# Kernel optimization log

Measured on AMD Instinct MI355X. Metric: run time of the kernel, lower is better.

Reference implementation:

```python
import jax, jax.numpy as jnp
import numpy as np

EPS = 1e-5
SLOPE = 0.2

def lrelu(x):
    return jnp.where(x > 0, x, SLOPE * x)

def bn_train(x, gamma, beta, axes):
    # training-mode batch norm over `axes`, channel dim = 1 (or features dim for 2D input)
    mean = jnp.mean(x, axis=axes, keepdims=True)
    var = jnp.mean((x - mean) ** 2, axis=axes, keepdims=True)
    sh = [1] * x.ndim
    sh[1] = -1
    return gamma.reshape(sh) * (x - mean) * jax.lax.rsqrt(var + EPS) + beta.reshape(sh)

def knn_sum(x, k):
    # x: (B, C, N). k-NN graph via pairwise squared distance, then sum of
    # gathered neighbor features over the k neighbors -> (B, C, N).
    inner = jnp.einsum('bcn,bcm->bnm', x, x)            # (B,N,N)
    sq = jnp.sum(x * x, axis=1)                          # (B,N)
    neg_dist = 2.0 * inner - sq[:, :, None] - sq[:, None, :]
    _, idx = jax.lax.top_k(neg_dist, k)                  # (B,N,k) nearest (incl. self)
    # gather: feat[b,c,n,j] = x[b,c,idx[b,n,j]]
    feat = jnp.take_along_axis(x[:, :, None, :], idx[:, None, :, :], axis=3)  # (B,C,N,k)
    return jnp.sum(feat, axis=3)

def edge_block(x, W, g, b, k):
    # get_graph_feature -> sum over neighbors -> conv1x1 -> BN -> LeakyReLU
    agg = knn_sum(x, k)                                  # (B,C,N)
    y = jnp.einsum('oc,bcn->bon', W, agg)                # 1x1 conv, no bias
    return lrelu(bn_train(y, g, b, (0, 2)))


def setup_inputs() -> dict:
    key = jax.random.key(0)
    ks = jax.random.split(key, 16)
    B, N, E, OUT = 16, 1024, 1024, 40
    w = lambda k_, sh, s=0.05: jax.random.normal(k_, sh, jnp.float32) * s
    ones = lambda n: jnp.ones((n,), jnp.float32)
    zeros = lambda n: jnp.zeros((n,), jnp.float32)
    return {
        'x': jax.random.normal(ks[0], (B, 3, N), jnp.float32),
        'W1': w(ks[1], (64, 3)),   'g1': ones(64),  'b1': zeros(64),
        'W2': w(ks[2], (64, 64)),  'g2': ones(64),  'b2': zeros(64),
        'W3': w(ks[3], (128, 64)), 'g3': ones(128), 'b3': zeros(128),
        'W4': w(ks[4], (256, 128)),'g4': ones(256), 'b4': zeros(256),
        'W5': w(ks[5], (E, 512)),  'g5': ones(E),   'b5': zeros(E),
        'lin1W': w(ks[6], (512, 2 * E)), 'g6': ones(512), 'b6': zeros(512),
        'lin2W': w(ks[7], (256, 512)), 'lin2b': zeros(256), 'g7': ones(256), 'b7': zeros(256),
        'lin3W': w(ks[8], (OUT, 256)), 'lin3b': zeros(OUT),
        'k': 20,
    }


def reference(x, W1, g1, b1, W2, g2, b2, W3, g3, b3, W4, g4, b4,
              W5, g5, b5, lin1W, g6, b6, lin2W, lin2b, g7, b7,
              lin3W, lin3b, k):
    x1 = edge_block(x,  W1, g1, b1, k)   # (B, 64, N)
    x2 = edge_block(x1, W2, g2, b2, k)   # (B, 64, N)
    x3 = edge_block(x2, W3, g3, b3, k)   # (B,128, N)
    x4 = edge_block(x3, W4, g4, b4, k)   # (B,256, N)
    h = jnp.concatenate([x1, x2, x3, x4], axis=1)        # (B,512,N)
    h = lrelu(bn_train(jnp.einsum('oc,bcn->bon', W5, h), g5, b5, (0, 2)))  # (B,E,N)
    hmax = jnp.max(h, axis=2)
    havg = jnp.mean(h, axis=2)
    z = jnp.concatenate([hmax, havg], axis=1)            # (B, 2E)
    z = lrelu(bn_train(z @ lin1W.T, g6, b6, (0,)))
    z = lrelu(bn_train(z @ lin2W.T + lin2b, g7, b7, (0,)))  # dropout = identity (eval)
    return z @ lin3W.T + lin3b                           # (B, 40)
```

## Files before the change

kernel.cpp:

```cpp
#include <hip/hip_runtime.h>
#include <hip/hip_bf16.h>
#include <math.h>

#define NPTS 1024
#define BATCH 16
#define KNN 20

typedef __attribute__((ext_vector_type(8))) short short8;
typedef __attribute__((ext_vector_type(4))) float f32x4;

__global__ __launch_bounds__(256) void compute_sq_kernel(const float* __restrict__ X,
    long batchStride, int C, float* __restrict__ sq) {
  const int b = blockIdx.y;
  const int m = blockIdx.x * 256 + threadIdx.x;
  const float* Xb = X + (long)b * batchStride;
  float s = 0.f;
  for (int c = 0; c < C; ++c) { float v = Xb[(long)c * NPTS + m]; s += v * v; }
  sq[b * NPTS + m] = s;
}

__global__ __launch_bounds__(256) void transpose_split_kernel(const float* __restrict__ in,
    long inBatchStride, int C, unsigned short* __restrict__ XH,
    unsigned short* __restrict__ XM, unsigned short* __restrict__ XL,
    float* __restrict__ XT) {
  __shared__ float tile[64][65];
  const int b  = blockIdx.z;
  const int n0 = blockIdx.x * 64, c0 = blockIdx.y * 64;
  const int tid = threadIdx.x;
  const float* ib = in + (long)b * inBatchStride;
  for (int i = tid; i < 4096; i += 256) {
    int r = i >> 6, cn = i & 63;
    tile[r][cn] = ib[(long)(c0 + r) * NPTS + n0 + cn];
  }
  __syncthreads();
  const long pb = (long)b * ((long)NPTS * C);
  for (int i = tid; i < 4096; i += 256) {
    int r = i >> 6, cc = i & 63;
    float f = tile[cc][r];
    __hip_bfloat16 h = __float2bfloat16(f);
    float r1 = f - __bfloat162float(h);
    __hip_bfloat16 m = __float2bfloat16(r1);
    float r2 = r1 - __bfloat162float(m);
    __hip_bfloat16 l = __float2bfloat16(r2);
    const long o = pb + (long)(n0 + r) * C + c0 + cc;
    XH[o] = *(unsigned short*)&h;
    XM[o] = *(unsigned short*)&m;
    XL[o] = *(unsigned short*)&l;
    XT[o] = f;
  }
}

template<int C>
__global__ __launch_bounds__(256) void knn_mfma_kernel(
    const unsigned short* __restrict__ XH, const unsigned short* __restrict__ XM,
    const unsigned short* __restrict__ XL, const float* __restrict__ sqg,
    float* __restrict__ PARTV, unsigned short* __restrict__ PARTI) {
  __shared__ __align__(16) unsigned short QP[6][64][40];
  __shared__ __align__(16) float Dbuf[64][68];
  float* region = (float*)&QP[0][0][0];

  const int b     = blockIdx.z;
  const int q0    = blockIdx.x * 64;
  const int p0    = blockIdx.y * 256;
  const int chunk = blockIdx.y;
  const int tid  = threadIdx.x;
  const int lane = tid & 63, w = tid >> 6;
  const int l16  = lane & 15, quad = lane >> 4;
  const int q = lane, sub = w;

  const long plane = (long)b * ((long)NPTS * C);
  const unsigned short* XHb = XH + plane;
  const unsigned short* XMb = XM + plane;
  const unsigned short* XLb = XL + plane;

  float sqw[4][4];
  #pragma unroll
  for (int pci = 0; pci < 4; ++pci)
    #pragma unroll
    for (int r = 0; r < 4; ++r)
      sqw[pci][r] = sqg[b * NPTS + p0 + pci * 64 + w * 16 + quad * 4 + r];

  float topv[KNN];
  int   topi[KNN];
  #pragma unroll
  for (int j = 0; j < KNN; ++j) { topv[j] = -INFINITY; topi[j] = 0x7fffffff; }
  float vmin = -INFINITY;

  const int srow = tid >> 2, sseg = (tid & 3) * 8;
  constexpr int KCN = C / 32;

  float4 rg0, rg1, rg2, rg3, rg4, rg5;
  {
    const long qo = (long)(q0 + srow) * C + sseg;
    const long po = (long)(p0 + srow) * C + sseg;
    rg0 = *(const float4*)&XHb[qo];
    rg1 = *(const float4*)&XMb[qo];
    rg2 = *(const float4*)&XLb[qo];
    rg3 = *(const float4*)&XHb[po];
    rg4 = *(const float4*)&XMb[po];
    rg5 = *(const float4*)&XLb[po];
  }

  for (int pci = 0; pci < 4; ++pci) {
    f32x4 acc[4];
    #pragma unroll
    for (int t = 0; t < 4; ++t) acc[t] = (f32x4){0.f, 0.f, 0.f, 0.f};

    for (int kci = 0; kci < KCN; ++kci) {
      __syncthreads();
      *(float4*)&QP[0][srow][sseg] = rg0;
      *(float4*)&QP[1][srow][sseg] = rg1;
      *(float4*)&QP[2][srow][sseg] = rg2;
      *(float4*)&QP[3][srow][sseg] = rg3;
      *(float4*)&QP[4][srow][sseg] = rg4;
      *(float4*)&QP[5][srow][sseg] = rg5;
      __syncthreads();
      const int ns = pci * KCN + kci + 1;
      if (ns < 4 * KCN) {
        const int npc = ns / KCN, nkc = (ns % KCN) * 32;
        const long qo = (long)(q0 + srow) * C + nkc + sseg;
        const long po = (long)(p0 + npc * 64 + srow) * C + nkc + sseg;
        rg0 = *(const float4*)&XHb[qo];
        rg1 = *(const float4*)&XMb[qo];
        rg2 = *(const float4*)&XLb[qo];
        rg3 = *(const float4*)&XHb[po];
        rg4 = *(const float4*)&XMb[po];
        rg5 = *(const float4*)&XLb[po];
      }
      const short8 ph = *(const short8*)&QP[3][w * 16 + l16][quad * 8];
      const short8 pm = *(const short8*)&QP[4][w * 16 + l16][quad * 8];
      const short8 pl = *(const short8*)&QP[5][w * 16 + l16][quad * 8];
      #pragma unroll
      for (int t = 0; t < 4; ++t) {
        const short8 qh = *(const short8*)&QP[0][t * 16 + l16][quad * 8];
        const short8 qm = *(const short8*)&QP[1][t * 16 + l16][quad * 8];
        const short8 ql = *(const short8*)&QP[2][t * 16 + l16][quad * 8];
        acc[t] = __builtin_amdgcn_mfma_f32_16x16x32_bf16(ph, qh, acc[t], 0, 0, 0);
        acc[t] = __builtin_amdgcn_mfma_f32_16x16x32_bf16(ph, qm, acc[t], 0, 0, 0);
        acc[t] = __builtin_amdgcn_mfma_f32_16x16x32_bf16(pm, qh, acc[t], 0, 0, 0);
        acc[t] = __builtin_amdgcn_mfma_f32_16x16x32_bf16(pm, qm, acc[t], 0, 0, 0);
        acc[t] = __builtin_amdgcn_mfma_f32_16x16x32_bf16(ph, ql, acc[t], 0, 0, 0);
        acc[t] = __builtin_amdgcn_mfma_f32_16x16x32_bf16(pl, qh, acc[t], 0, 0, 0);
      }
    }
    #pragma unroll
    for (int t = 0; t < 4; ++t)
      #pragma unroll
      for (int r = 0; r < 4; ++r)
        Dbuf[w * 16 + quad * 4 + r][t * 16 + l16] = fmaf(2.f, acc[t][r], -sqw[pci][r]);
    __syncthreads();

    #pragma unroll 4
    for (int i = 0; i < 16; ++i) {
      const float v = Dbuf[sub * 16 + i][q];
      if (v > vmin) {
        float cv = v; int ci = p0 + pci * 64 + sub * 16 + i;
        bool ins = false;
        #pragma unroll
        for (int j = 0; j < KNN; ++j) {
          const float tv = topv[j]; const int ti = topi[j];
          const bool gt = ins || (cv > tv);
          topv[j] = gt ? cv : tv;
          topi[j] = gt ? ci : ti;
          cv = gt ? tv : cv;
          ci = gt ? ti : ci;
          ins = gt;
        }
        vmin = topv[KNN - 1];
      }
    }
  }

  __syncthreads();
  {
    float* mv = region;
    unsigned short* mi = (unsigned short*)(region + 5120);
    const int slot = q * 4 + sub;
    #pragma unroll
    for (int j = 0; j < KNN; ++j) { mv[j * 256 + slot] = topv[j]; mi[j * 256 + slot] = (unsigned short)topi[j]; }
  }
  __syncthreads();
  if (tid < 64) {
    const float* mv = region;
    const unsigned short* mi = (const unsigned short*)(region + 5120);
    int p0_ = 0, p1 = 0, p2 = 0, p3 = 0;
    float* opv = PARTV + (((long)(b * NPTS + q0 + tid)) * 4 + chunk) * KNN;
    unsigned short* opi = PARTI + (((long)(b * NPTS + q0 + tid)) * 4 + chunk) * KNN;
    for (int j = 0; j < KNN; ++j) {
      float bv = -INFINITY; int bi = 0x7fffffff; int bs = 0;
      if (p0_ < KNN) { float v = mv[p0_ * 256 + tid * 4 + 0]; int i = mi[p0_ * 256 + tid * 4 + 0];
        if (v > bv || (v == bv && i < bi)) { bv = v; bi = i; bs = 0; } }
      if (p1 < KNN) { float v = mv[p1 * 256 + tid * 4 + 1]; int i = mi[p1 * 256 + tid * 4 + 1];
        if (v > bv || (v == bv && i < bi)) { bv = v; bi = i; bs = 1; } }
      if (p2 < KNN) { float v = mv[p2 * 256 + tid * 4 + 2]; int i = mi[p2 * 256 + tid * 4 + 2];
        if (v > bv || (v == bv && i < bi)) { bv = v; bi = i; bs = 2; } }
      if (p3 < KNN) { float v = mv[p3 * 256 + tid * 4 + 3]; int i = mi[p3 * 256 + tid * 4 + 3];
        if (v > bv || (v == bv && i < bi)) { bv = v; bi = i; bs = 3; } }
      p0_ += (bs == 0); p1 += (bs == 1); p2 += (bs == 2); p3 += (bs == 3);
      opv[j] = bv; opi[j] = (unsigned short)bi;
    }
  }
}

template<int C>
__global__ __launch_bounds__(256) void knn_kernel(const float* __restrict__ X,
    long batchStride, const float* __restrict__ sqg,
    float* __restrict__ PARTV, unsigned short* __restrict__ PARTI) {
  constexpr int CT = (C < 64) ? C : 64;
  constexpr int REGF = (2 * CT * 64 > 7680) ? 2 * CT * 64 : 7680;
  __shared__ float Dbuf[64][68];
  __shared__ float region[REGF];

  float* qbuf = region;
  float* pbuf = region + CT * 64;

  const int b     = blockIdx.z;
  const int q0    = blockIdx.x * 64;
  const int p0    = blockIdx.y * 256;
  const int chunk = blockIdx.y;
  const int tid = threadIdx.x;
  const int ty  = tid >> 4, tx = tid & 15;
  const int q   = tid & 63;
  const int sub = tid >> 6;
  const float* Xb = X + (long)b * batchStride;
  const float* sqb = sqg + b * NPTS;

  float topv[KNN];
  int   topi[KNN];
  #pragma unroll
  for (int j = 0; j < KNN; ++j) { topv[j] = -INFINITY; topi[j] = 0x7fffffff; }
  float vmin = -INFINITY;

  for (int pc = p0; pc < p0 + 256; pc += 64) {
    float acc[4][4] = {};
    for (int cc = 0; cc < C; cc += CT) {
      __syncthreads();
      for (int t = tid; t < 64 * CT; t += 256) {
        int c = t >> 6, m = t & 63;
        qbuf[c * 64 + m] = Xb[(long)(cc + c) * NPTS + q0 + m];
        pbuf[c * 64 + m] = Xb[(long)(cc + c) * NPTS + pc + m];
      }
      __syncthreads();
      #pragma unroll
      for (int c = 0; c < CT; ++c) {
        const float4 qv = *(const float4*)&qbuf[c * 64 + ty * 4];
        const float4 pv = *(const float4*)&pbuf[c * 64 + tx * 4];
        acc[0][0] += qv.x * pv.x; acc[0][1] += qv.x * pv.y; acc[0][2] += qv.x * pv.z; acc[0][3] += qv.x * pv.w;
        acc[1][0] += qv.y * pv.x; acc[1][1] += qv.y * pv.y; acc[1][2] += qv.y * pv.z; acc[1][3] += qv.y * pv.w;
        acc[2][0] += qv.z * pv.x; acc[2][1] += qv.z * pv.y; acc[2][2] += qv.z * pv.z; acc[2][3] += qv.z * pv.w;
        acc[3][0] += qv.w * pv.x; acc[3][1] += qv.w * pv.y; acc[3][2] += qv.w * pv.z; acc[3][3] += qv.w * pv.w;
      }
    }
    #pragma unroll
    for (int j = 0; j < 4; ++j) {
      const int p = pc + tx * 4 + j;
      const float sq = sqb[p];
      float4 dv;
      dv.x = 2.f * acc[0][j] - sq;
      dv.y = 2.f * acc[1][j] - sq;
      dv.z = 2.f * acc[2][j] - sq;
      dv.w = 2.f * acc[3][j] - sq;
      *(float4*)&Dbuf[tx * 4 + j][ty * 4] = dv;
    }
    __syncthreads();

    #pragma unroll 4
    for (int i = 0; i < 16; ++i) {
      const float v = Dbuf[sub * 16 + i][q];
      if (v > vmin) {
        float cv = v; int ci = pc + sub * 16 + i;
        bool ins = false;
        #pragma unroll
        for (int j = 0; j < KNN; ++j) {
          const float tv = topv[j]; const int ti = topi[j];
          const bool gt = ins || (cv > tv);
          topv[j] = gt ? cv : tv;
          topi[j] = gt ? ci : ti;
          cv = gt ? tv : cv;
          ci = gt ? ti : ci;
          ins = gt;
        }
        vmin = topv[KNN - 1];
      }
    }
  }

  __syncthreads();
  {
    float* mv = region;
    unsigned short* mi = (unsigned short*)(region + 5120);
    const int slot = q * 4 + sub;
    #pragma unroll
    for (int j = 0; j < KNN; ++j) { mv[j * 256 + slot] = topv[j]; mi[j * 256 + slot] = (unsigned short)topi[j]; }
  }
  __syncthreads();
  if (tid < 64) {
    const float* mv = region;
    const unsigned short* mi = (const unsigned short*)(region + 5120);
    int p0_ = 0, p1 = 0, p2 = 0, p3 = 0;
    float* opv = PARTV + (((long)(b * NPTS + q0 + tid)) * 4 + chunk) * KNN;
    unsigned short* opi = PARTI + (((long)(b * NPTS + q0 + tid)) * 4 + chunk) * KNN;
    for (int j = 0; j < KNN; ++j) {
      float bv = -INFINITY; int bi = 0x7fffffff; int bs = 0;
      if (p0_ < KNN) { float v = mv[p0_ * 256 + tid * 4 + 0]; int i = mi[p0_ * 256 + tid * 4 + 0];
        if (v > bv || (v == bv && i < bi)) { bv = v; bi = i; bs = 0; } }
      if (p1 < KNN) { float v = mv[p1 * 256 + tid * 4 + 1]; int i = mi[p1 * 256 + tid * 4 + 1];
        if (v > bv || (v == bv && i < bi)) { bv = v; bi = i; bs = 1; } }
      if (p2 < KNN) { float v = mv[p2 * 256 + tid * 4 + 2]; int i = mi[p2 * 256 + tid * 4 + 2];
        if (v > bv || (v == bv && i < bi)) { bv = v; bi = i; bs = 2; } }
      if (p3 < KNN) { float v = mv[p3 * 256 + tid * 4 + 3]; int i = mi[p3 * 256 + tid * 4 + 3];
        if (v > bv || (v == bv && i < bi)) { bv = v; bi = i; bs = 3; } }
      p0_ += (bs == 0); p1 += (bs == 1); p2 += (bs == 2); p3 += (bs == 3);
      opv[j] = bv; opi[j] = (unsigned short)bi;
    }
  }
}

__global__ __launch_bounds__(256) void knn_merge_kernel(const float* __restrict__ PARTV,
    const unsigned short* __restrict__ PARTI, int* __restrict__ idxOut) {
  const int idx = blockIdx.x * 256 + threadIdx.x;
  const float* pv = PARTV + (long)idx * 4 * KNN;
  const unsigned short* pi = PARTI + (long)idx * 4 * KNN;
  int p0 = 0, p1 = 0, p2 = 0, p3 = 0;
  int* op = idxOut + (long)idx * KNN;
  for (int j = 0; j < KNN; ++j) {
    float bv = -INFINITY; int bi = 0x7fffffff; int bs = 0;
    if (p0 < KNN) { float v = pv[0 * KNN + p0]; int i = pi[0 * KNN + p0];
      if (v > bv || (v == bv && i < bi)) { bv = v; bi = i; bs = 0; } }
    if (p1 < KNN) { float v = pv[1 * KNN + p1]; int i = pi[1 * KNN + p1];
      if (v > bv || (v == bv && i < bi)) { bv = v; bi = i; bs = 1; } }
    if (p2 < KNN) { float v = pv[2 * KNN + p2]; int i = pi[2 * KNN + p2];
      if (v > bv || (v == bv && i < bi)) { bv = v; bi = i; bs = 2; } }
    if (p3 < KNN) { float v = pv[3 * KNN + p3]; int i = pi[3 * KNN + p3];
      if (v > bv || (v == bv && i < bi)) { bv = v; bi = i; bs = 3; } }
    p0 += (bs == 0); p1 += (bs == 1); p2 += (bs == 2); p3 += (bs == 3);
    op[j] = bi;
  }
}

__global__ __launch_bounds__(256) void gather_sum_kernel(const float* __restrict__ X,
    long batchStride, int C, const int* __restrict__ idx, float* __restrict__ agg) {
  __shared__ int sidx[256][KNN + 1];
  const int b     = blockIdx.z;
  const int n0    = blockIdx.x * 256;
  const int cbase = blockIdx.y * 8;
  const int tid   = threadIdx.x;
  const int* ib = idx + ((long)(b * NPTS + n0)) * KNN;
  for (int t = tid; t < 256 * KNN; t += 256) {
    sidx[t / KNN][t % KNN] = ib[t];
  }
  __syncthreads();
  const float* Xb = X + (long)b * batchStride;
  float* ab = agg + (long)b * C * NPTS;
  const int cend = min(cbase + 8, C);
  for (int c = cbase; c < cend; ++c) {
    const float* row = Xb + (long)c * NPTS;
    float s = 0.f;
    #pragma unroll
    for (int j = 0; j < KNN; ++j) s += row[sidx[tid][j]];
    ab[(long)c * NPTS + n0 + tid] = s;
  }
}

__global__ __launch_bounds__(256) void gather_sum_vec_kernel(const float* __restrict__ XT,
    int C, const int* __restrict__ idx, float* __restrict__ agg) {
  __shared__ int sidx[256][KNN + 1];
  const int b     = blockIdx.z;
  const int n0    = blockIdx.x * 256;
  const int cbase = blockIdx.y * 16;
  const int tid   = threadIdx.x;
  const int* ib = idx + ((long)(b * NPTS + n0)) * KNN;
  for (int t = tid; t < 256 * KNN; t += 256) {
    sidx[t / KNN][t % KNN] = ib[t];
  }
  __syncthreads();
  const float* Xb = XT + (long)b * ((long)NPTS * C);
  float* ab = agg + (long)b * C * NPTS;
  const int cend = min(cbase + 16, C);
  for (int c = cbase; c < cend; c += 8) {
    float a0 = 0.f, a1 = 0.f, a2 = 0.f, a3 = 0.f, a4 = 0.f, a5 = 0.f, a6 = 0.f, a7 = 0.f;
    #pragma unroll
    for (int j = 0; j < KNN; ++j) {
      const float* rp = Xb + (long)sidx[tid][j] * C + c;
      const float4 v0 = *(const float4*)rp;
      const float4 v1 = *(const float4*)(rp + 4);
      a0 += v0.x; a1 += v0.y; a2 += v0.z; a3 += v0.w;
      a4 += v1.x; a5 += v1.y; a6 += v1.z; a7 += v1.w;
    }
    float* op = ab + (long)c * NPTS + n0 + tid;
    op[0 * NPTS] = a0; op[1 * NPTS] = a1; op[2 * NPTS] = a2; op[3 * NPTS] = a3;
    op[4 * NPTS] = a4; op[5 * NPTS] = a5; op[6 * NPTS] = a6; op[7 * NPTS] = a7;
  }
}

__global__ __launch_bounds__(256) void conv_kernel(const float* __restrict__ Xin, long inBatchStride,
    const float* __restrict__ W, int C, int O,
    float* __restrict__ Yout, long outBatchStride, int outChanOffset) {
  __shared__ float Wt[32][68];
  __shared__ float Xt[32][68];
  const int b   = blockIdx.z;
  const int o0  = blockIdx.y * 64;
  const int n0  = blockIdx.x * 64;
  const int tid = threadIdx.x;
  const int ty  = tid >> 4, tx = tid & 15;
  const float* Xb = Xin + (long)b * inBatchStride;
  float acc[4][4] = {};
  for (int cc = 0; cc < C; cc += 32) {
    const int cw = min(32, C - cc);
    __syncthreads();
    for (int t = tid; t < 64 * 32; t += 256) {
      int oo = t >> 5, kk = t & 31;
      Wt[kk][oo] = (kk < cw) ? W[(long)(o0 + oo) * C + cc + kk] : 0.f;
    }
    for (int t = tid; t < 32 * 64; t += 256) {
      int kk = t >> 6, nn = t & 63;
      Xt[kk][nn] = (kk < cw) ? Xb[(long)(cc + kk) * NPTS + n0 + nn] : 0.f;
    }
    __syncthreads();
    #pragma unroll
    for (int kk = 0; kk < 32; ++kk) {
      const float4 wv = *(const float4*)&Wt[kk][ty * 4];
      const float4 xv = *(const float4*)&Xt[kk][tx * 4];
      acc[0][0] += wv.x * xv.x; acc[0][1] += wv.x * xv.y; acc[0][2] += wv.x * xv.z; acc[0][3] += wv.x * xv.w;
      acc[1][0] += wv.y * xv.x; acc[1][1] += wv.y * xv.y; acc[1][2] += wv.y * xv.z; acc[1][3] += wv.y * xv.w;
      acc[2][0] += wv.z * xv.x; acc[2][1] += wv.z * xv.y; acc[2][2] += wv.z * xv.z; acc[2][3] += wv.z * xv.w;
      acc[3][0] += wv.w * xv.x; acc[3][1] += wv.w * xv.y; acc[3][2] += wv.w * xv.z; acc[3][3] += wv.w * xv.w;
    }
  }
  #pragma unroll
  for (int i = 0; i < 4; ++i) {
    float4 v = make_float4(acc[i][0], acc[i][1], acc[i][2], acc[i][3]);
    *(float4*)&Yout[(long)b * outBatchStride + (long)(outChanOffset + o0 + ty * 4 + i) * NPTS + n0 + tx * 4] = v;
  }
}

__global__ __launch_bounds__(256) void transpose_bf16_kernel(const float* __restrict__ in,
    long inBatchStride, int C, unsigned short* __restrict__ outT) {
  __shared__ float tile[64][65];
  const int b  = blockIdx.z;
  const int n0 = blockIdx.x * 64, c0 = blockIdx.y * 64;
  const int tid = threadIdx.x;
  const float* ib = in + (long)b * inBatchStride;
  for (int i = tid; i < 4096; i += 256) {
    int r = i >> 6, cn = i & 63;
    tile[r][cn] = ib[(long)(c0 + r) * NPTS + n0 + cn];
  }
  __syncthreads();
  unsigned short* ob = outT + (long)b * ((long)NPTS * C);
  for (int i = tid; i < 4096; i += 256) {
    int r = i >> 6, cc = i & 63;
    __hip_bfloat16 h = __float2bfloat16(tile[cc][r]);
    ob[(long)(n0 + r) * C + c0 + cc] = *(unsigned short*)&h;
  }
}

__global__ void convert_bf16_kernel(const float* __restrict__ in,
                                    unsigned short* __restrict__ out, int n) {
  int i = blockIdx.x * 256 + threadIdx.x;
  if (i < n) { __hip_bfloat16 h = __float2bfloat16(in[i]); out[i] = *(unsigned short*)&h; }
}

__global__ __launch_bounds__(256) void conv_mfma_kernel(const unsigned short* __restrict__ Wbf,
    const unsigned short* __restrict__ XT, int C,
    float* __restrict__ Yout, long outBatchStride, int outChanOffset) {
  __shared__ unsigned short Wl[128][40];
  __shared__ unsigned short Xl[128][40];
  const int b  = blockIdx.z;
  const int o0 = blockIdx.y * 128;
  const int n0 = blockIdx.x * 128;
  const int tid  = threadIdx.x;
  const int lane = tid & 63, wid = tid >> 6;
  const int wo = (wid >> 1) * 64, wn = (wid & 1) * 64;
  const int l16 = lane & 15, quad = lane >> 4;
  const unsigned short* Wg = Wbf + (long)o0 * C;
  const unsigned short* Xg = XT + (long)b * ((long)NPTS * C) + (long)n0 * C;

  f32x4 acc[4][4];
  #pragma unroll
  for (int i = 0; i < 4; ++i)
    #pragma unroll
    for (int j = 0; j < 4; ++j) acc[i][j] = (f32x4){0.f, 0.f, 0.f, 0.f};

  for (int kk = 0; kk < C; kk += 32) {
    __syncthreads();
    #pragma unroll
    for (int it = 0; it < 2; ++it) {
      const int id = tid + it * 256;
      const int r = id >> 2, qq = id & 3;
      const float4 va = *(const float4*)&Wg[(long)r * C + kk + qq * 8];
      const float4 vb = *(const float4*)&Xg[(long)r * C + kk + qq * 8];
      *(float4*)&Wl[r][qq * 8] = va;
      *(float4*)&Xl[r][qq * 8] = vb;
    }
    __syncthreads();
    short8 af[4], bfr[4];
    #pragma unroll
    for (int i = 0; i < 4; ++i) af[i]  = *(const short8*)&Wl[wo + i * 16 + l16][quad * 8];
    #pragma unroll
    for (int j = 0; j < 4; ++j) bfr[j] = *(const short8*)&Xl[wn + j * 16 + l16][quad * 8];
    #pragma unroll
    for (int i = 0; i < 4; ++i)
      #pragma unroll
      for (int j = 0; j < 4; ++j)
        acc[i][j] = __builtin_amdgcn_mfma_f32_16x16x32_bf16(af[i], bfr[j], acc[i][j], 0, 0, 0);
  }

  float* Yb = Yout + (long)b * outBatchStride + (long)outChanOffset * NPTS;
  #pragma unroll
  for (int i = 0; i < 4; ++i) {
    #pragma unroll
    for (int r = 0; r < 4; ++r) {
      const int o = o0 + wo + i * 16 + quad * 4 + r;
      float* row = Yb + (long)o * NPTS + n0 + wn;
      #pragma unroll
      for (int j = 0; j < 4; ++j) row[j * 16 + l16] = acc[i][j][r];
    }
  }
}

__global__ __launch_bounds__(256) void bn_stats_kernel(const float* __restrict__ Y, long batchStride,
    int chanOffset, float* __restrict__ meanOut, float* __restrict__ rstdOut) {
  const int o   = blockIdx.x;
  const int tid = threadIdx.x;
  const float* base = Y + (long)(chanOffset + o) * NPTS;
  float s = 0.f, s2 = 0.f;
  for (int b = 0; b < BATCH; ++b) {
    const float* p = base + (long)b * batchStride;
    for (int t = tid; t < NPTS; t += 256) { float v = p[t]; s += v; s2 += v * v; }
  }
  for (int off = 32; off > 0; off >>= 1) { s += __shfl_down(s, off); s2 += __shfl_down(s2, off); }
  __shared__ float r1[4], r2[4];
  const int wid = tid >> 6;
  if ((tid & 63) == 0) { r1[wid] = s; r2[wid] = s2; }
  __syncthreads();
  if (tid == 0) {
    s  = r1[0] + r1[1] + r1[2] + r1[3];
    s2 = r2[0] + r2[1] + r2[2] + r2[3];
    float m   = s * (1.f / 16384.f);
    float var = s2 * (1.f / 16384.f) - m * m;
    meanOut[o] = m;
    rstdOut[o] = rsqrtf(var + 1e-5f);
  }
}

__global__ __launch_bounds__(256) void bn_apply_kernel(float* __restrict__ Y, long batchStride, int chanOffset,
    const float* __restrict__ meanB, const float* __restrict__ rstdB,
    const float* __restrict__ g, const float* __restrict__ beta) {
  const int n = blockIdx.x * 256 + threadIdx.x;
  const int o = blockIdx.y;
  const int b = blockIdx.z;
  float* p = Y + (long)b * batchStride + (long)(chanOffset + o) * NPTS;
  const float sc = rstdB[o] * g[o];
  float v = (p[n] - meanB[o]) * sc + beta[o];
  p[n] = (v > 0.f) ? v : 0.2f * v;
}

__global__ __launch_bounds__(256) void bn_pool_kernel(const float* __restrict__ H,
    const float* __restrict__ meanB, const float* __restrict__ rstdB,
    const float* __restrict__ g, const float* __restrict__ beta,
    float* __restrict__ Z) {
  const int o   = blockIdx.x;
  const int b   = blockIdx.y;
  const int tid = threadIdx.x;
  const float* p = H + (long)b * (1024L * NPTS) + (long)o * NPTS;
  const float sc = rstdB[o] * g[o], mu = meanB[o], bb = beta[o];
  float mx = -INFINITY, s = 0.f;
  for (int t = tid; t < NPTS; t += 256) {
    float v = (p[t] - mu) * sc + bb;
    v = (v > 0.f) ? v : 0.2f * v;
    mx = fmaxf(mx, v);
    s += v;
  }
  for (int off = 32; off > 0; off >>= 1) { mx = fmaxf(mx, __shfl_down(mx, off)); s += __shfl_down(s, off); }
  __shared__ float rm[4], rs[4];
  const int wid = tid >> 6;
  if ((tid & 63) == 0) { rm[wid] = mx; rs[wid] = s; }
  __syncthreads();
  if (tid == 0) {
    mx = fmaxf(fmaxf(rm[0], rm[1]), fmaxf(rm[2], rm[3]));
    s  = rs[0] + rs[1] + rs[2] + rs[3];
    Z[(long)b * 2048 + o]        = mx;
    Z[(long)b * 2048 + 1024 + o] = s * (1.f / 1024.f);
  }
}

__global__ __launch_bounds__(256) void fc_wave_kernel(const float* __restrict__ in,
    const float* __restrict__ Wm, const float* __restrict__ bias,
    float* __restrict__ out, int Cin, int Oout) {
  const int wid  = threadIdx.x >> 6;
  const int lane = threadIdx.x & 63;
  const int o = blockIdx.x * 4 + wid;
  if (o >= Oout) return;
  const float* wp = Wm + (long)o * Cin;
  float acc[BATCH];
  #pragma unroll
  for (int b = 0; b < BATCH; ++b) acc[b] = 0.f;
  for (int c = lane; c < Cin; c += 64) {
    const float w = wp[c];
    #pragma unroll
    for (int b = 0; b < BATCH; ++b) acc[b] += w * in[b * Cin + c];
  }
  #pragma unroll
  for (int b = 0; b < BATCH; ++b) {
    #pragma unroll
    for (int off = 32; off > 0; off >>= 1) acc[b] += __shfl_down(acc[b], off);
  }
  if (lane == 0) {
    const float bs = bias ? bias[o] : 0.f;
    #pragma unroll
    for (int b = 0; b < BATCH; ++b) out[b * Oout + o] = acc[b] + bs;
  }
}

__global__ void bn_small_kernel(float* __restrict__ buf, const float* __restrict__ g,
    const float* __restrict__ beta, int O) {
  const int o = blockIdx.x * 256 + threadIdx.x;
  if (o >= O) return;
  float s = 0.f, s2 = 0.f;
  for (int b = 0; b < BATCH; ++b) { float v = buf[b * O + o]; s += v; s2 += v * v; }
  const float m   = s * (1.f / 16.f);
  const float var = s2 * (1.f / 16.f) - m * m;
  const float sc  = rsqrtf(var + 1e-5f) * g[o];
  const float bb  = beta[o];
  for (int b = 0; b < BATCH; ++b) {
    float v = (buf[b * O + o] - m) * sc + bb;
    buf[b * O + o] = (v > 0.f) ? v : 0.2f * v;
  }
}

extern "C" void kernel_launch(void* const* d_in, const int* in_sizes, int n_in,
                              void* d_out, int out_size, void* d_ws, size_t ws_size,
                              hipStream_t stream) {
  const float* x   = (const float*)d_in[0];
  const float* W1  = (const float*)d_in[1];
  const float* g1  = (const float*)d_in[2];
  const float* b1  = (const float*)d_in[3];
  const float* W2  = (const float*)d_in[4];
  const float* g2  = (const float*)d_in[5];
  const float* b2  = (const float*)d_in[6];
  const float* W3  = (const float*)d_in[7];
  const float* g3  = (const float*)d_in[8];
  const float* b3  = (const float*)d_in[9];
  const float* W4  = (const float*)d_in[10];
  const float* g4  = (const float*)d_in[11];
  const float* b4  = (const float*)d_in[12];
  const float* W5  = (const float*)d_in[13];
  const float* g5  = (const float*)d_in[14];
  const float* b5  = (const float*)d_in[15];
  const float* l1W = (const float*)d_in[16];
  const float* g6  = (const float*)d_in[17];
  const float* b6  = (const float*)d_in[18];
  const float* l2W = (const float*)d_in[19];
  const float* l2b = (const float*)d_in[20];
  const float* g7  = (const float*)d_in[21];
  const float* b7  = (const float*)d_in[22];
  const float* l3W = (const float*)d_in[23];
  const float* l3b = (const float*)d_in[24];

  float* ws   = (float*)d_ws;
  float* Xcat = ws;
  float* H    = Xcat + 8388608;
  float* REG  = H + 16777216;
  float* AGG  = REG;
  unsigned short* AGGT = (unsigned short*)(REG + 2097152);
  unsigned short* XbfT = (unsigned short*)REG;
  int*   IDX  = (int*)(REG + 4194304);
  float* MEAN = (float*)(IDX + 327680);
  float* RSTD = MEAN + 1024;
  float* Z    = RSTD + 1024;
  float* Z1   = Z + 32768;
  float* Z2   = Z1 + 8192;
  unsigned short* W4bf = (unsigned short*)(Z2 + 4096);
  unsigned short* W5bf = W4bf + 32768;

  float* SQ    = H;
  float* PARTV = H + 16384;
  unsigned short* PARTI = (unsigned short*)(PARTV + 1310720);
  unsigned short* XH = (unsigned short*)(H + 1982464);
  unsigned short* XM = (unsigned short*)(H + 1982464 + 1048576);
  unsigned short* XL = (unsigned short*)(H + 1982464 + 2097152);
  float* XTf = H + 1982464 + 3145728;

  const long XS = 512L * 1024;
  const long HS = 1024L * 1024;
  const dim3 knnGrid(16, 4, 16);

  compute_sq_kernel<<<dim3(4, 16), 256, 0, stream>>>(x, 3L * 1024, 3, SQ);
  knn_kernel<3><<<knnGrid, 256, 0, stream>>>(x, 3L * 1024, SQ, PARTV, PARTI);
  knn_merge_kernel<<<64, 256, 0, stream>>>(PARTV, PARTI, IDX);
  gather_sum_kernel<<<dim3(4, 1, 16), 256, 0, stream>>>(x, 3L * 1024, 3, IDX, AGG);
  conv_kernel<<<dim3(16, 1, 16), 256, 0, stream>>>(AGG, 3L * 1024, W1, 3, 64, Xcat, XS, 0);
  bn_stats_kernel<<<64, 256, 0, stream>>>(Xcat, XS, 0, MEAN, RSTD);
  bn_apply_kernel<<<dim3(4, 64, 16), 256, 0, stream>>>(Xcat, XS, 0, MEAN, RSTD, g1, b1);

  compute_sq_kernel<<<dim3(4, 16), 256, 0, stream>>>(Xcat, XS, 64, SQ);
  transpose_split_kernel<<<dim3(16, 1, 16), 256, 0, stream>>>(Xcat, XS, 64, XH, XM, XL, XTf);
  knn_mfma_kernel<64><<<knnGrid, 256, 0, stream>>>(XH, XM, XL, SQ, PARTV, PARTI);
  knn_merge_kernel<<<64, 256, 0, stream>>>(PARTV, PARTI, IDX);
  gather_sum_vec_kernel<<<dim3(4, 4, 16), 256, 0, stream>>>(XTf, 64, IDX, AGG);
  conv_kernel<<<dim3(16, 1, 16), 256, 0, stream>>>(AGG, 64L * 1024, W2, 64, 64, Xcat, XS, 64);
  bn_stats_kernel<<<64, 256, 0, stream>>>(Xcat, XS, 64, MEAN, RSTD);
  bn_apply_kernel<<<dim3(4, 64, 16), 256, 0, stream>>>(Xcat, XS, 64, MEAN, RSTD, g2, b2);

  compute_sq_kernel<<<dim3(4, 16), 256, 0, stream>>>(Xcat + 64L * 1024, XS, 64, SQ);
  transpose_split_kernel<<<dim3(16, 1, 16), 256, 0, stream>>>(Xcat + 64L * 1024, XS, 64, XH, XM, XL, XTf);
  knn_mfma_kernel<64><<<knnGrid, 256, 0, stream>>>(XH, XM, XL, SQ, PARTV, PARTI);
  knn_merge_kernel<<<64, 256, 0, stream>>>(PARTV, PARTI, IDX);
  gather_sum_vec_kernel<<<dim3(4, 4, 16), 256, 0, stream>>>(XTf, 64, IDX, AGG);
  conv_kernel<<<dim3(16, 2, 16), 256, 0, stream>>>(AGG, 64L * 1024, W3, 64, 128, Xcat, XS, 128);
  bn_stats_kernel<<<128, 256, 0, stream>>>(Xcat, XS, 128, MEAN, RSTD);
  bn_apply_kernel<<<dim3(4, 128, 16), 256, 0, stream>>>(Xcat, XS, 128, MEAN, RSTD, g3, b3);

  compute_sq_kernel<<<dim3(4, 16), 256, 0, stream>>>(Xcat + 128L * 1024, XS, 128, SQ);
  transpose_split_kernel<<<dim3(16, 2, 16), 256, 0, stream>>>(Xcat + 128L * 1024, XS, 128, XH, XM, XL, XTf);
  knn_mfma_kernel<128><<<knnGrid, 256, 0, stream>>>(XH, XM, XL, SQ, PARTV, PARTI);
  knn_merge_kernel<<<64, 256, 0, stream>>>(PARTV, PARTI, IDX);
  gather_sum_vec_kernel<<<dim3(4, 8, 16), 256, 0, stream>>>(XTf, 128, IDX, AGG);
  convert_bf16_kernel<<<128, 256, 0, stream>>>(W4, W4bf, 256 * 128);
  transpose_bf16_kernel<<<dim3(16, 2, 16), 256, 0, stream>>>(AGG, 128L * 1024, 128, AGGT);
  conv_mfma_kernel<<<dim3(8, 2, 16), 256, 0, stream>>>(W4bf, AGGT, 128, Xcat, XS, 256);
  bn_stats_kernel<<<256, 256, 0, stream>>>(Xcat, XS, 256, MEAN, RSTD);
  bn_apply_kernel<<<dim3(4, 256, 16), 256, 0, stream>>>(Xcat, XS, 256, MEAN, RSTD, g4, b4);

  convert_bf16_kernel<<<2048, 256, 0, stream>>>(W5, W5bf, 1024 * 512);
  transpose_bf16_kernel<<<dim3(16, 8, 16), 256, 0, stream>>>(Xcat, XS, 512, XbfT);
  conv_mfma_kernel<<<dim3(8, 8, 16), 256, 0, stream>>>(W5bf, XbfT, 512, H, HS, 0);
  bn_stats_kernel<<<1024, 256, 0, stream>>>(H, HS, 0, MEAN, RSTD);
  bn_pool_kernel<<<dim3(1024, 16), 256, 0, stream>>>(H, MEAN, RSTD, g5, b5, Z);

  fc_wave_kernel<<<128, 256, 0, stream>>>(Z, l1W, nullptr, Z1, 2048, 512);
  bn_small_kernel<<<2, 256, 0, stream>>>(Z1, g6, b6, 512);
  fc_wave_kernel<<<64, 256, 0, stream>>>(Z1, l2W, l2b, Z2, 512, 256);
  bn_small_kernel<<<1, 256, 0, stream>>>(Z2, g7, b7, 256);
  fc_wave_kernel<<<10, 256, 0, stream>>>(Z2, l3W, l3b, (float*)d_out, 256, 40);
}
```

Measured before the change: 1.025 ms.

## Overlay distance buffer onto shared tiles and use rank-based top-k insertion

The distance tile buffer in both kNN kernels now aliases existing shared-memory regions (the MFMA query/point staging area, and a fixed region in the small-C kernel). This cuts LDS use per block so more blocks can be resident, at the price of an extra barrier before the tile is written. The sorted insertion is replaced by a helper that counts the insert position by comparison and shifts with selects, which shortens the serial dependency chain. Ties now place a new equal value after existing ones, and the small-C kernel gains a static_assert limiting it to C<=3.

```diff
diff --git a/kernel.cpp b/kernel.cpp
--- a/kernel.cpp
+++ b/kernel.cpp
@@ -8,6 +8,22 @@
 
 typedef __attribute__((ext_vector_type(8))) short short8;
 typedef __attribute__((ext_vector_type(4))) float f32x4;
+
+__device__ __forceinline__ void topk_insert(float (&topv)[KNN], int (&topi)[KNN],
+                                            float v, int ci, float& vmin) {
+  int pos = 0;
+  #pragma unroll
+  for (int j = 0; j < KNN; ++j) pos += (topv[j] >= v) ? 1 : 0;
+  #pragma unroll
+  for (int j = KNN - 1; j > 0; --j) {
+    const bool keep = (j < pos);
+    const bool ins  = (j == pos);
+    topv[j] = keep ? topv[j] : (ins ? v  : topv[j - 1]);
+    topi[j] = keep ? topi[j] : (ins ? ci : topi[j - 1]);
+  }
+  if (pos == 0) { topv[0] = v; topi[0] = ci; }
+  vmin = topv[KNN - 1];
+}
 
 __global__ __launch_bounds__(256) void compute_sq_kernel(const float* __restrict__ X,
     long batchStride, int C, float* __restrict__ sq) {
@@ -56,7 +72,7 @@
     const unsigned short* __restrict__ XL, const float* __restrict__ sqg,
     float* __restrict__ PARTV, unsigned short* __restrict__ PARTI) {
   __shared__ __align__(16) unsigned short QP[6][64][40];
-  __shared__ __align__(16) float Dbuf[64][68];
+  float* Dbuf   = (float*)&QP[0][0][0];
   float* region = (float*)&QP[0][0][0];
 
   const int b     = blockIdx.z;
@@ -143,31 +159,18 @@
         acc[t] = __builtin_amdgcn_mfma_f32_16x16x32_bf16(pl, qh, acc[t], 0, 0, 0);
       }
     }
+    __syncthreads();
     #pragma unroll
     for (int t = 0; t < 4; ++t)
       #pragma unroll
       for (int r = 0; r < 4; ++r)
-        Dbuf[w * 16 + quad * 4 + r][t * 16 + l16] = fmaf(2.f, acc[t][r], -sqw[pci][r]);
+        Dbuf[(w * 16 + quad * 4 + r) * 68 + t * 16 + l16] = fmaf(2.f, acc[t][r], -sqw[pci][r]);
     __syncthreads();
 
     #pragma unroll 4
     for (int i = 0; i < 16; ++i) {
-      const float v = Dbuf[sub * 16 + i][q];
-      if (v > vmin) {
-        float cv = v; int ci = p0 + pci * 64 + sub * 16 + i;
-        bool ins = false;
-        #pragma unroll
-        for (int j = 0; j < KNN; ++j) {
-          const float tv = topv[j]; const int ti = topi[j];
-          const bool gt = ins || (cv > tv);
-          topv[j] = gt ? cv : tv;
-          topi[j] = gt ? ci : ti;
-          cv = gt ? tv : cv;
-          ci = gt ? ti : ci;
-          ins = gt;
-        }
-        vmin = topv[KNN - 1];
-      }
+      const float v = Dbuf[(sub * 16 + i) * 68 + q];
+      if (v > vmin) topk_insert(topv, topi, v, p0 + pci * 64 + sub * 16 + i, vmin);
     }
   }
 
@@ -206,13 +209,11 @@
 __global__ __launch_bounds__(256) void knn_kernel(const float* __restrict__ X,
     long batchStride, const float* __restrict__ sqg,
     float* __restrict__ PARTV, unsigned short* __restrict__ PARTI) {
-  constexpr int CT = (C < 64) ? C : 64;
-  constexpr int REGF = (2 * CT * 64 > 7680) ? 2 * CT * 64 : 7680;
-  __shared__ float Dbuf[64][68];
-  __shared__ float region[REGF];
-
+  static_assert(C <= 3, "overlay layout assumes tiny C");
+  __shared__ float region[7680];
   float* qbuf = region;
-  float* pbuf = region + CT * 64;
+  float* pbuf = region + C * 64;
+  float* Dbuf = region + 512;
 
   const int b     = blockIdx.z;
   const int q0    = blockIdx.x * 64;
@@ -233,16 +234,16 @@
 
   for (int pc = p0; pc < p0 + 256; pc += 64) {
     float acc[4][4] = {};
-    for (int cc = 0; cc < C; cc += CT) {
+    {
       __syncthreads();
-      for (int t = tid; t < 64 * CT; t += 256) {
+      for (int t = tid; t < 64 * C; t += 256) {
         int c = t >> 6, m = t & 63;
-        qbuf[c * 64 + m] = Xb[(long)(cc + c) * NPTS + q0 + m];
-        pbuf[c * 64 + m] = Xb[(long)(cc + c) * NPTS + pc + m];
+        qbuf[c * 64 + m] = Xb[(long)c * NPTS + q0 + m];
+        pbuf[c * 64 + m] = Xb[(long)c * NPTS + pc + m];
       }
       __syncthreads();
       #pragma unroll
-      for (int c = 0; c < CT; ++c) {
+      for (int c = 0; c < C; ++c) {
         const float4 qv = *(const float4*)&qbuf[c * 64 + ty * 4];
         const float4 pv = *(const float4*)&pbuf[c * 64 + tx * 4];
         acc[0][0] += qv.x * pv.x; acc[0][1] += qv.x * pv.y; acc[0][2] += qv.x * pv.z; acc[0][3] += qv.x * pv.w;
@@ -260,28 +261,14 @@
       dv.y = 2.f * acc[1][j] - sq;
       dv.z = 2.f * acc[2][j] - sq;
       dv.w = 2.f * acc[3][j] - sq;
-      *(float4*)&Dbuf[tx * 4 + j][ty * 4] = dv;
+      *(float4*)&Dbuf[(tx * 4 + j) * 68 + ty * 4] = dv;
     }
     __syncthreads();
 
     #pragma unroll 4
     for (int i = 0; i < 16; ++i) {
-      const float v = Dbuf[sub * 16 + i][q];
-      if (v > vmin) {
-        float cv = v; int ci = pc + sub * 16 + i;
-        bool ins = false;
-        #pragma unroll
-        for (int j = 0; j < KNN; ++j) {
-          const float tv = topv[j]; const int ti = topi[j];
-          const bool gt = ins || (cv > tv);
-          topv[j] = gt ? cv : tv;
-          topi[j] = gt ? ci : ti;
-          cv = gt ? tv : cv;
-          ci = gt ? ti : ci;
-          ins = gt;
-        }
-        vmin = topv[KNN - 1];
-      }
+      const float v = Dbuf[(sub * 16 + i) * 68 + q];
+      if (v > vmin) topk_insert(topv, topi, v, pc + sub * 16 + i, vmin);
     }
   }
 
```

Result: slower. 1.059 ms (+3.3%).
